# Kernel optimization log

Hardware: AMD Instinct MI355X
Metric: run time of the kernel (lower is better)

## Reference

```python
import jax, jax.numpy as jnp
import numpy as np

N = 40000   # query points
M = 40000   # support points
H = 32      # neighbors per query
CIN = 64
COUT = 64
KS = 3      # kernel points per dim
PDIM = 3
K = KS ** PDIM  # 27 kernel points
RADIUS = 1.0
KP_EXTENT = RADIUS / (KS - 1) * PDIM ** 0.5


def _kernel_points():
    # replicates KPConv.getKernelPoints: grid of KS^PDIM points in a ball of RADIUS
    xyz = np.linspace(-1.0, 1.0, KS)
    pts = np.meshgrid(*PDIM * [xyz])
    pts = np.vstack([p.flatten() for p in pts]).T  # [K, PDIM]
    pts = pts / PDIM ** 0.5
    return (pts * RADIUS).astype(np.float32)


def setup_inputs() -> dict:
    key = jax.random.key(0)
    k1, k2, k3, k4, k5 = jax.random.split(key, 5)
    q_pts = jax.random.uniform(k1, (N, PDIM), dtype=jnp.float32) * 10.0
    s_pts = jax.random.uniform(k2, (M, PDIM), dtype=jnp.float32) * 10.0
    neighb_inds = jax.random.randint(k3, (N, H), 0, M + 1)  # M == shadow index
    x = jax.random.normal(k4, (M, CIN), dtype=jnp.float32)
    # kaiming-uniform-like init for weights [K, CIN, COUT]
    bound = (6.0 / ((1.0 + 5.0) * CIN)) ** 0.5
    weights = jax.random.uniform(k5, (K, CIN, COUT), dtype=jnp.float32,
                                 minval=-bound, maxval=bound)
    kernel_points = jnp.asarray(_kernel_points())
    return {"q_pts": q_pts, "s_pts": s_pts, "neighb_inds": neighb_inds,
            "x": x, "weights": weights, "kernel_points": kernel_points}


def reference(q_pts, s_pts, neighb_inds, x, weights, kernel_points):
    # append shadow support point (far away) and zero shadow feature
    s_pts_p = jnp.concatenate(
        [s_pts, jnp.full((1, s_pts.shape[-1]), 1e6, dtype=s_pts.dtype)], axis=0)
    x_p = jnp.concatenate(
        [x, jnp.zeros((1, x.shape[-1]), dtype=x.dtype)], axis=0)

    neighbors = s_pts_p[neighb_inds] - q_pts[:, None, :]        # [N, H, 3]
    neighb_x = x_p[neighb_inds]                                  # [N, H, CIN]

    # distance of each neighbor to each kernel point
    diff = neighbors[:, :, None, :] - kernel_points              # [N, H, K, 3]
    sq_d = jnp.sum(diff * diff, axis=-1)                         # [N, H, K]
    all_w = jnp.clip(1.0 - jnp.sqrt(sq_d) / KP_EXTENT, 0.0)      # [N, H, K]

    # all_weights^T @ neighb_x  -> [N, K, CIN]
    weighted = jnp.einsum('nhk,nhc->nkc', all_w, neighb_x)
    # per-kernel-point matmul with weights [K, CIN, COUT], summed over K
    out = jnp.einsum('nkc,kco->no', weighted, weights)           # [N, COUT]
    return out
```

## Files before the change

kernel.cpp:

```cpp
#include <hip/hip_runtime.h>

typedef short bf16x8 __attribute__((ext_vector_type(8)));
typedef float f32x4  __attribute__((ext_vector_type(4)));

#define HN    32
#define CIN   64
#define KP    27
#define QB    64
#define CAPB  96
#define NTB   1024
#define OSTR  65

#define QB2   64
#define CAP2  128
#define OSTR2 68

#define INV_EXT 1.1547005383792517f
#define CUT2    3.4821f

__device__ __forceinline__ unsigned f2bf(float f){
    union{float fv;unsigned u;}v; v.fv=f;
    unsigned u=v.u;
    u += 0x7fffu + ((u>>16)&1u);
    return u>>16;
}

__global__ void pack_spts(const float* __restrict__ s, float4* __restrict__ o, int M){
    int i = blockIdx.x*256 + threadIdx.x;
    if (i < M) o[i] = make_float4(s[i*3+0], s[i*3+1], s[i*3+2], 0.f);
}

__global__ void pack_wt2(const float* __restrict__ W, unsigned short* __restrict__ Wt2){
    int tid = blockIdx.x*256 + threadIdx.x;
    if (tid >= KP*8*64) return;
    int lane = tid & 63;
    int f  = (tid>>6) & 7;
    int k  = tid >> 9;
    int ot = f>>1, ks = f&1, g = lane>>4;
    unsigned r[8];
#pragma unroll
    for (int j=0;j<8;++j)
        r[j] = f2bf(W[(size_t)k*4096 + (size_t)(ks*32 + g*8 + j)*64 + ot*16 + (lane&15)]);
    uint4 v; v.x=r[0]|(r[1]<<16); v.y=r[2]|(r[3]<<16); v.z=r[4]|(r[5]<<16); v.w=r[6]|(r[7]<<16);
    *(uint4*)&Wt2[(size_t)tid*8] = v;
}

__global__ __launch_bounds__(256)
void kp_prep2(const float* __restrict__ s, const float* __restrict__ W,
              float4* __restrict__ o, unsigned short* __restrict__ Wt2, int M)
{
    int tid = blockIdx.x*256 + threadIdx.x;
    if (tid < M) o[tid] = make_float4(s[tid*3+0], s[tid*3+1], s[tid*3+2], 0.f);
    if (tid < KP*8*64){
        int lane = tid & 63;
        int f  = (tid>>6) & 7;
        int kk = tid >> 9;
        int ot = f>>1, ks = f&1, gg = lane>>4;
        unsigned r[8];
#pragma unroll
        for (int j=0;j<8;++j)
            r[j] = f2bf(W[(size_t)kk*4096 + (size_t)(ks*32 + gg*8 + j)*64 + ot*16 + (lane&15)]);
        uint4 v; v.x=r[0]|(r[1]<<16); v.y=r[2]|(r[3]<<16); v.z=r[4]|(r[5]<<16); v.w=r[6]|(r[7]<<16);
        *(uint4*)&Wt2[(size_t)tid*8] = v;
    }
}

__device__ __forceinline__ void loadB(const unsigned short* __restrict__ Wt2, int k, int lane,
                                      bf16x8 (&b)[8]){
    const unsigned short* base = Wt2 + ((size_t)(k*8)*64 + lane)*8;
#pragma unroll
    for (int f=0;f<8;++f) b[f] = *(const bf16x8*)(base + f*512);
}
__device__ __forceinline__ bf16x8 ldBf(const unsigned short* __restrict__ Wt2, int k, int f, int lane){
    return *(const bf16x8*)(Wt2 + ((size_t)(k*8 + f)*64 + lane)*8);
}
__device__ __forceinline__ void loadB_w(const float* __restrict__ W, int k, int lane, int g,
                                        bf16x8 (&b)[8]){
#pragma unroll
    for (int f=0;f<8;++f){
        int ot=f>>1, ks=f&1;
        union{unsigned u[4]; bf16x8 v;} bb;
#pragma unroll
        for (int jj=0;jj<4;++jj){
            unsigned l0=f2bf(W[(size_t)k*4096 + (size_t)(ks*32+g*8+2*jj)*64   + ot*16+(lane&15)]);
            unsigned l1=f2bf(W[(size_t)k*4096 + (size_t)(ks*32+g*8+2*jj+1)*64 + ot*16+(lane&15)]);
            bb.u[jj]=l0|(l1<<16);
        }
        b[f]=bb.v;
    }
}

__global__ __launch_bounds__(256,4)
void kpconv_fused(const float* __restrict__ q_pts, const int* __restrict__ inds,
                  const float* __restrict__ x, const float* __restrict__ kpts,
                  const float4* __restrict__ sp4, const unsigned short* __restrict__ Wt2,
                  float* __restrict__ out, int N, int M)
{
    __shared__ unsigned short rows[64*CIN];
    __shared__ __align__(16) float wlds[KP*64];
    __shared__ __align__(16) float outacc[QB2*OSTR2];
    __shared__ float qls[QB2*3];
    __shared__ float bx[CAP2], by[CAP2], bz[CAP2];
    __shared__ __align__(16) int bq[CAP2];
    __shared__ int bixs[CAP2];
    __shared__ int cnt;

    const int t    = threadIdx.x;
    const int lane = t & 63;
    const int wv   = t >> 6;
    const int g    = lane >> 4;
    const int r15  = lane & 15;
    const int nq0  = blockIdx.x * QB2;
    const int NP   = N*HN;

    for (int j=t; j<QB2*OSTR2; j+=256) outacc[j]=0.f;
    for (int j=t; j<QB2*3;    j+=256){ int gi=nq0*3+j; qls[j]=(gi<N*3)? q_pts[gi]:0.f; }
    if (t < CAP2) bq[t]=0;
    if (t==0) cnt=0;
    __syncthreads();

#pragma unroll
    for (int jj=0; jj<8; ++jj){
        int pl   = jj*256 + t;
        int pair = nq0*HN + pl;
        if (pair < NP){
            int idx = inds[pair];
            if ((unsigned)idx < (unsigned)M){
                int q = pl >> 5;
                float4 s4 = sp4[idx];
                float px=s4.x-qls[q*3], py=s4.y-qls[q*3+1], pz=s4.z-qls[q*3+2];
                if (px*px+py*py+pz*pz <= CUT2){
                    int sl = atomicAdd(&cnt, 1);
                    if (sl < CAP2){ bx[sl]=px; by[sl]=py; bz[sl]=pz; bq[sl]=q; bixs[sl]=idx; }
                }
            }
        }
    }
    __syncthreads();
    const int total = cnt;

    auto processTile = [&](int base, int cc){
        for (int it=t; it<64*8; it+=256){
            int rl=it>>3, c8=it&7, e=base+rl;
            uint4 v; v.x=0u; v.y=0u; v.z=0u; v.w=0u;
            if (e < cc){
                int ix = bixs[e];
                const float4* xr = (const float4*)(x + (size_t)ix*CIN);
                float4 f0=xr[c8*2], f1=xr[c8*2+1];
                v.x=f2bf(f0.x)|(f2bf(f0.y)<<16); v.y=f2bf(f0.z)|(f2bf(f0.w)<<16);
                v.z=f2bf(f1.x)|(f2bf(f1.y)<<16); v.w=f2bf(f1.z)|(f2bf(f1.w)<<16);
            }
            int ba = rl*128 + ((c8*16)^((rl&7)<<4));
            *(uint4*)((char*)rows+ba) = v;
        }
        for (int i=t; i<KP*64; i+=256){
            int k=i>>6, row=i&63, e=base+row;
            float w=0.f;
            if (e < cc){
                float dx=bx[e]-kpts[k*3+0];
                float dy=by[e]-kpts[k*3+1];
                float dz=bz[e]-kpts[k*3+2];
                w = fmaxf(1.f - sqrtf(dx*dx+dy*dy+dz*dz)*INV_EXT, 0.f);
            }
            wlds[i]=w;
        }
        __syncthreads();

        const char* rb = (const char*)rows;
        bf16x8 A0[4], A1[4];
#pragma unroll
        for (int rt=0; rt<4; ++rt){
            int row = rt*16 + r15;
            A0[rt] = *(const bf16x8*)(rb + row*128 + (( g*16)    ^((row&7)<<4)));
            A1[rt] = *(const bf16x8*)(rb + row*128 + ((64+g*16)  ^((row&7)<<4)));
        }
        f32x4 acc[4];
#pragma unroll
        for (int rt=0; rt<4; ++rt){ acc[rt][0]=0.f; acc[rt][1]=0.f; acc[rt][2]=0.f; acc[rt][3]=0.f; }

        const int f0 = wv*2, f1 = wv*2+1;
        bf16x8 Bc0 = ldBf(Wt2, 0, f0, lane);
        bf16x8 Bc1 = ldBf(Wt2, 0, f1, lane);
#pragma unroll 1
        for (int k=0; k<KP; ++k){
            int kn = (k+1 < KP) ? (k+1) : k;
            bf16x8 Bn0 = ldBf(Wt2, kn, f0, lane);
            bf16x8 Bn1 = ldBf(Wt2, kn, f1, lane);
            const float* wk = &wlds[k*64];
#pragma unroll
            for (int rt=0; rt<4; ++rt){
                f32x4 w4 = *(const f32x4*)(wk + rt*16 + g*4);
                bool act = (w4[0]>0.f)|(w4[1]>0.f)|(w4[2]>0.f)|(w4[3]>0.f);
                if (__any(act)){
                    f32x4 c; c[0]=0.f; c[1]=0.f; c[2]=0.f; c[3]=0.f;
                    c = __builtin_amdgcn_mfma_f32_16x16x32_bf16(A0[rt], Bc0, c, 0,0,0);
                    c = __builtin_amdgcn_mfma_f32_16x16x32_bf16(A1[rt], Bc1, c, 0,0,0);
                    acc[rt][0] += w4[0]*c[0];
                    acc[rt][1] += w4[1]*c[1];
                    acc[rt][2] += w4[2]*c[2];
                    acc[rt][3] += w4[3]*c[3];
                }
            }
            Bc0 = Bn0; Bc1 = Bn1;
        }
#pragma unroll
        for (int rt=0; rt<4; ++rt){
            int4 q4 = *(const int4*)&bq[base + rt*16 + g*4];
#pragma unroll
            for (int rr=0; rr<4; ++rr){
                float val = acc[rt][rr];
                int qv = (rr==0)? q4.x : (rr==1)? q4.y : (rr==2)? q4.z : q4.w;
                if (val != 0.f)
                    atomicAdd(&outacc[qv*OSTR2 + wv*16 + r15], val);
            }
        }
        __syncthreads();
    };

    if (total <= CAP2){
        int nt = (total + 63) >> 6;
        for (int tile=0; tile<nt; ++tile) processTile(tile*64, total);
    } else {
        for (int w=0; w<(QB2*HN)/64; ++w){
            __syncthreads();
            if (t==0) cnt=0;
            __syncthreads();
            if (t < 64){
                int pl = w*64 + t, pair = nq0*HN + pl;
                if (pair < NP){
                    int idx = inds[pair];
                    if ((unsigned)idx < (unsigned)M){
                        int q = pl >> 5;
                        float4 s4 = sp4[idx];
                        float px=s4.x-qls[q*3], py=s4.y-qls[q*3+1], pz=s4.z-qls[q*3+2];
                        if (px*px+py*py+pz*pz <= CUT2){
                            int sl = atomicAdd(&cnt, 1);
                            bx[sl]=px; by[sl]=py; bz[sl]=pz; bq[sl]=q; bixs[sl]=idx;
                        }
                    }
                }
            }
            __syncthreads();
            if (cnt > 0) processTile(0, cnt);
        }
    }
    __syncthreads();

    for (int j=t; j<QB2*16; j+=256){
        int q=j>>4, o4=j&15, n=nq0+q;
        if (n < N)
            ((float4*)out)[(size_t)n*16 + o4] = *(const float4*)&outacc[q*OSTR2 + o4*4];
    }
}


__global__ __launch_bounds__(NTB)
void kpconv6(const float* __restrict__ q_pts, const float* __restrict__ s_pts,
             const int* __restrict__ inds, const float* __restrict__ x,
             const float* __restrict__ W, const float* __restrict__ kpts,
             const float4* __restrict__ sp4, const unsigned short* __restrict__ Wt2,
             int use_ws, float* __restrict__ out, int N, int M)
{
    __shared__ float qls[QB*3];
    __shared__ float posx[CAPB], posy[CAPB], posz[CAPB];
    __shared__ int   eqb[CAPB], eidxb[CAPB];
    __shared__ unsigned short rows[CAPB*CIN];
    __shared__ float outacc[QB*OSTR];
    __shared__ int   cnt;

    const int t    = threadIdx.x;
    const int lane = t & 63;
    const int wv   = t >> 6;
    const int g    = lane >> 4;
    const int r15  = lane & 15;
    const int nq0  = blockIdx.x * QB;

    const int k0 = wv, k1 = wv + 16;
    const bool has2 = (k1 < KP);

    bf16x8 B0[8], B1[8];
    if (use_ws){
        loadB(Wt2, k0, lane, B0);
        loadB(Wt2, has2 ? k1 : k0, lane, B1);
    } else {
        loadB_w(W, k0, lane, g, B0);
        loadB_w(W, has2 ? k1 : k0, lane, g, B1);
    }
    const float k0x=kpts[k0*3+0], k0y=kpts[k0*3+1], k0z=kpts[k0*3+2];
    float k1x=0.f,k1y=0.f,k1z=0.f;
    if (has2){ k1x=kpts[k1*3+0]; k1y=kpts[k1*3+1]; k1z=kpts[k1*3+2]; }

    for (int j=t; j<QB*OSTR; j+=NTB) outacc[j]=0.f;
    for (int j=t; j<QB*3;   j+=NTB){ int gi=nq0*3+j; qls[j]=(gi<N*3)? q_pts[gi]:0.f; }
    if (t==0) cnt=0;
    __syncthreads();

    auto process = [&](int cc){
        if (cc<=0) return;
        const int ntile=(cc+15)>>4, nrow=ntile*16;
        for (int j=cc+t; j<nrow; j+=NTB){ posx[j]=1e9f; posy[j]=1e9f; posz[j]=1e9f; eqb[j]=0; }
        for (int it=t; it<nrow*8; it+=NTB){
            int e=it>>3, c8=it&7;
            uint4 v; v.x=0u; v.y=0u; v.z=0u; v.w=0u;
            if (e<cc){
                const float4* xr=(const float4*)(x+(size_t)eidxb[e]*CIN);
                float4 f0=xr[c8*2], f1=xr[c8*2+1];
                v.x=f2bf(f0.x)|(f2bf(f0.y)<<16); v.y=f2bf(f0.z)|(f2bf(f0.w)<<16);
                v.z=f2bf(f1.x)|(f2bf(f1.y)<<16); v.w=f2bf(f1.z)|(f2bf(f1.w)<<16);
            }
            int ba=e*128+((c8*16)^((e&7)<<4));
            *(uint4*)((char*)rows+ba)=v;
        }
        __syncthreads();
        for (int tile=0; tile<ntile; ++tile){
            const char* rb=(const char*)rows;
            int row=tile*16+r15;
            bf16x8 a0=*(const bf16x8*)(rb+row*128+((g*16)    ^((row&7)<<4)));
            bf16x8 a1=*(const bf16x8*)(rb+row*128+((64+g*16) ^((row&7)<<4)));
            int rbase=tile*16+g*4;
            float w0[4], w1[4]; int qq[4];
#pragma unroll
            for (int r=0;r<4;++r){
                float sx=posx[rbase+r], sy=posy[rbase+r], sz=posz[rbase+r];
                qq[r]=eqb[rbase+r];
                float dx=sx-k0x, dy=sy-k0y, dz=sz-k0z;
                w0[r]=fmaxf(1.f-sqrtf(dx*dx+dy*dy+dz*dz)*INV_EXT,0.f);
                float ex=sx-k1x, ey=sy-k1y, ez=sz-k1z;
                float w1r=fmaxf(1.f-sqrtf(ex*ex+ey*ey+ez*ez)*INV_EXT,0.f);
                w1[r]=has2? w1r : 0.f;
            }
#pragma unroll
            for (int ot=0;ot<4;++ot){
                f32x4 c={0.f,0.f,0.f,0.f};
                c=__builtin_amdgcn_mfma_f32_16x16x32_bf16(a0,B0[2*ot],c,0,0,0);
                c=__builtin_amdgcn_mfma_f32_16x16x32_bf16(a1,B0[2*ot+1],c,0,0,0);
                f32x4 d={0.f,0.f,0.f,0.f};
                if (has2){
                    d=__builtin_amdgcn_mfma_f32_16x16x32_bf16(a0,B1[2*ot],d,0,0,0);
                    d=__builtin_amdgcn_mfma_f32_16x16x32_bf16(a1,B1[2*ot+1],d,0,0,0);
                }
#pragma unroll
                for (int r=0;r<4;++r){
                    float val=w0[r]*c[r]+w1[r]*d[r];
                    if (val!=0.f) atomicAdd(&outacc[qq[r]*OSTR+ot*16+r15], val);
                }
            }
        }
        __syncthreads();
    };

    for (int it=t; it<QB*HN; it+=NTB){
        int q=it>>5, h=it&31, n=nq0+q;
        bool inr=false; int idx=0; float px=0.f,py=0.f,pz=0.f;
        if (n<N){
            idx=inds[(size_t)n*HN+h];
            if ((unsigned)idx<(unsigned)M){
                float sx,sy,sz;
                if (use_ws){ float4 s4=sp4[idx]; sx=s4.x; sy=s4.y; sz=s4.z; }
                else { sx=s_pts[idx*3]; sy=s_pts[idx*3+1]; sz=s_pts[idx*3+2]; }
                px=sx-qls[q*3]; py=sy-qls[q*3+1]; pz=sz-qls[q*3+2];
                inr=(px*px+py*py+pz*pz)<=CUT2;
            }
        }
        if (inr){
            int sl=atomicAdd(&cnt,1);
            if (sl<CAPB){ eqb[sl]=q; eidxb[sl]=idx; posx[sl]=px; posy[sl]=py; posz[sl]=pz; }
        }
    }
    __syncthreads();
    const int total=cnt;

    if (total<=CAPB){
        process(total);
    } else {
        for (int w=0; w<(QB*HN)/64; ++w){
            __syncthreads();
            if (t==0) cnt=0;
            __syncthreads();
            if (t<64){
                int pair=w*64+t;
                int q=pair>>5, h=pair&31, n=nq0+q;
                if (n<N){
                    int idx=inds[(size_t)n*HN+h];
                    if ((unsigned)idx<(unsigned)M){
                        float sx,sy,sz;
                        if (use_ws){ float4 s4=sp4[idx]; sx=s4.x; sy=s4.y; sz=s4.z; }
                        else { sx=s_pts[idx*3]; sy=s_pts[idx*3+1]; sz=s_pts[idx*3+2]; }
                        float px=sx-qls[q*3], py=sy-qls[q*3+1], pz=sz-qls[q*3+2];
                        if (px*px+py*py+pz*pz<=CUT2){
                            int sl=atomicAdd(&cnt,1);
                            eqb[sl]=q; eidxb[sl]=idx; posx[sl]=px; posy[sl]=py; posz[sl]=pz;
                        }
                    }
                }
            }
            __syncthreads();
            process(cnt);
        }
    }
    __syncthreads();

    for (int j=t; j<QB*CIN; j+=NTB){
        int q=j>>6, o=j&63, n=nq0+q;
        if (n<N) out[(size_t)n*CIN+o]=outacc[q*OSTR+o];
    }
}

extern "C" void kernel_launch(void* const* d_in, const int* in_sizes, int n_in,
                              void* d_out, int out_size, void* d_ws, size_t ws_size,
                              hipStream_t stream)
{
    const float* q_pts=(const float*)d_in[0];
    const float* s_pts=(const float*)d_in[1];
    const int*   inds =(const int*)d_in[2];
    const float* x    =(const float*)d_in[3];
    const float* W    =(const float*)d_in[4];
    const float* kpts =(const float*)d_in[5];
    float* outp=(float*)d_out;
    int N=in_sizes[0]/3;
    int M=in_sizes[1]/3;

    char* wsb=(char*)d_ws;
    float4* sp4=(float4*)wsb;
    unsigned short* Wt2=(unsigned short*)(wsb + (size_t)M*16);

    const size_t WT2B = (size_t)KP*8*64*8*2;
    size_t need = (size_t)M*16 + WT2B;

    if (ws_size >= need){
        int prepN = (M > KP*8*64) ? M : KP*8*64;
        hipLaunchKernelGGL(kp_prep2, dim3((prepN+255)/256), dim3(256), 0, stream,
                           s_pts, W, sp4, Wt2, M);
        int nblocks = (N + QB2 - 1) / QB2;
        hipLaunchKernelGGL(kpconv_fused, dim3(nblocks), dim3(256), 0, stream,
                           q_pts, inds, x, kpts, sp4, Wt2, outp, N, M);
        return;
    }

    hipLaunchKernelGGL(kpconv6, dim3((N+QB-1)/QB), dim3(NTB), 0, stream,
                       q_pts, s_pts, inds, x, W, kpts, sp4, Wt2, 0, outp, N, M);
}
```

Baseline: 44.82 us.

## Halve query block, size tile to valid rows, and skip empty row tiles

Cuts the queries per block from 64 to 32 and the candidate capacity from 128 to 64, so one tile always covers the filtered neighbors. processTile now gathers features, computes kernel-point weights and runs MFMA only for the 16-row groups that hold valid entries. The weight prefetch is hoisted ahead of the gather. It also raises the launch-bounds occupancy hint to 5 waves. The aim is less padded work and more resident blocks, at the cost of twice as many blocks, each reloading the full weight set.

Result: faster. 41.34 us, median of 2 (-7.8%).

```diff
diff --git a/kernel.cpp b/kernel.cpp
--- a/kernel.cpp
+++ b/kernel.cpp
@@ -11,8 +11,8 @@
 #define NTB   1024
 #define OSTR  65
 
-#define QB2   64
-#define CAP2  128
+#define QB2   32
+#define CAP2  64
 #define OSTR2 68
 
 #define INV_EXT 1.1547005383792517f
@@ -90,7 +90,7 @@
     }
 }
 
-__global__ __launch_bounds__(256,4)
+__global__ __launch_bounds__(256,5)
 void kpconv_fused(const float* __restrict__ q_pts, const int* __restrict__ inds,
                   const float* __restrict__ x, const float* __restrict__ kpts,
                   const float4* __restrict__ sp4, const unsigned short* __restrict__ Wt2,
@@ -120,7 +120,7 @@
     __syncthreads();
 
 #pragma unroll
-    for (int jj=0; jj<8; ++jj){
+    for (int jj=0; jj<4; ++jj){
         int pl   = jj*256 + t;
         int pair = nq0*HN + pl;
         if (pair < NP){
@@ -139,27 +139,33 @@
     __syncthreads();
     const int total = cnt;
 
-    auto processTile = [&](int base, int cc){
-        for (int it=t; it<64*8; it+=256){
-            int rl=it>>3, c8=it&7, e=base+rl;
+    auto processTile = [&](int cc){
+        const int nrow = (cc + 15) & ~15;
+        const int f0 = wv*2, f1 = wv*2+1;
+        bf16x8 Bc0 = ldBf(Wt2, 0, f0, lane);
+        bf16x8 Bc1 = ldBf(Wt2, 0, f1, lane);
+        for (int it=t; it<nrow*8; it+=256){
+            int rl=it>>3, c8=it&7;
             uint4 v; v.x=0u; v.y=0u; v.z=0u; v.w=0u;
-            if (e < cc){
-                int ix = bixs[e];
+            if (rl < cc){
+                int ix = bixs[rl];
                 const float4* xr = (const float4*)(x + (size_t)ix*CIN);
-                float4 f0=xr[c8*2], f1=xr[c8*2+1];
-                v.x=f2bf(f0.x)|(f2bf(f0.y)<<16); v.y=f2bf(f0.z)|(f2bf(f0.w)<<16);
-                v.z=f2bf(f1.x)|(f2bf(f1.y)<<16); v.w=f2bf(f1.z)|(f2bf(f1.w)<<16);
+                float4 fr0=xr[c8*2], fr1=xr[c8*2+1];
+                v.x=f2bf(fr0.x)|(f2bf(fr0.y)<<16); v.y=f2bf(fr0.z)|(f2bf(fr0.w)<<16);
+                v.z=f2bf(fr1.x)|(f2bf(fr1.y)<<16); v.w=f2bf(fr1.z)|(f2bf(fr1.w)<<16);
             }
             int ba = rl*128 + ((c8*16)^((rl&7)<<4));
             *(uint4*)((char*)rows+ba) = v;
         }
         for (int i=t; i<KP*64; i+=256){
-            int k=i>>6, row=i&63, e=base+row;
+            int row = i&63;
+            if (row >= nrow) continue;
+            int k = i>>6;
             float w=0.f;
-            if (e < cc){
-                float dx=bx[e]-kpts[k*3+0];
-                float dy=by[e]-kpts[k*3+1];
-                float dz=bz[e]-kpts[k*3+2];
+            if (row < cc){
+                float dx=bx[row]-kpts[k*3+0];
+                float dy=by[row]-kpts[k*3+1];
+                float dz=bz[row]-kpts[k*3+2];
                 w = fmaxf(1.f - sqrtf(dx*dx+dy*dy+dz*dz)*INV_EXT, 0.f);
             }
             wlds[i]=w;
@@ -170,6 +176,7 @@
         bf16x8 A0[4], A1[4];
 #pragma unroll
         for (int rt=0; rt<4; ++rt){
+            if (rt*16 >= cc) continue;
             int row = rt*16 + r15;
             A0[rt] = *(const bf16x8*)(rb + row*128 + (( g*16)    ^((row&7)<<4)));
             A1[rt] = *(const bf16x8*)(rb + row*128 + ((64+g*16)  ^((row&7)<<4)));
@@ -178,9 +185,6 @@
 #pragma unroll
         for (int rt=0; rt<4; ++rt){ acc[rt][0]=0.f; acc[rt][1]=0.f; acc[rt][2]=0.f; acc[rt][3]=0.f; }
 
-        const int f0 = wv*2, f1 = wv*2+1;
-        bf16x8 Bc0 = ldBf(Wt2, 0, f0, lane);
-        bf16x8 Bc1 = ldBf(Wt2, 0, f1, lane);
 #pragma unroll 1
         for (int k=0; k<KP; ++k){
             int kn = (k+1 < KP) ? (k+1) : k;
@@ -189,6 +193,7 @@
             const float* wk = &wlds[k*64];
 #pragma unroll
             for (int rt=0; rt<4; ++rt){
+                if (rt*16 >= cc) continue;
                 f32x4 w4 = *(const f32x4*)(wk + rt*16 + g*4);
                 bool act = (w4[0]>0.f)|(w4[1]>0.f)|(w4[2]>0.f)|(w4[3]>0.f);
                 if (__any(act)){
@@ -205,7 +210,8 @@
         }
 #pragma unroll
         for (int rt=0; rt<4; ++rt){
-            int4 q4 = *(const int4*)&bq[base + rt*16 + g*4];
+            if (rt*16 >= cc) continue;
+            int4 q4 = *(const int4*)&bq[rt*16 + g*4];
 #pragma unroll
             for (int rr=0; rr<4; ++rr){
                 float val = acc[rt][rr];
@@ -218,8 +224,7 @@
     };
 
     if (total <= CAP2){
-        int nt = (total + 63) >> 6;
-        for (int tile=0; tile<nt; ++tile) processTile(tile*64, total);
+        if (total > 0) processTile(total);
     } else {
         for (int w=0; w<(QB2*HN)/64; ++w){
             __syncthreads();
@@ -241,7 +246,7 @@
                 }
             }
             __syncthreads();
-            if (cnt > 0) processTile(0, cnt);
+            if (cnt > 0) processTile(cnt);
         }
     }
     __syncthreads();
```
